# Performance work log

Measured on AMD Instinct MI355X. Metric: run time of the kernel, lower is better.

Reference implementation:

```python
import jax, jax.numpy as jnp
import numpy as np


def _cheb_conv(x, row, col, norm, W, b, num_nodes):
    # PyG ChebConv with sym normalization and lambda_max=2:
    # L_hat = -D^{-1/2} A D^{-1/2} (off-diagonal), diagonal exactly 0.
    # Tx_0 = x; Tx_1 = L_hat x; Tx_k = 2 L_hat Tx_{k-1} - Tx_{k-2}
    K = W.shape[0]
    Tx0 = x
    out = Tx0 @ W[0]
    Tx1 = jax.ops.segment_sum(norm[:, None] * Tx0[col], row, num_segments=num_nodes)
    out = out + Tx1 @ W[1]
    for k in range(2, K):
        Tx2 = 2.0 * jax.ops.segment_sum(norm[:, None] * Tx1[col], row, num_segments=num_nodes) - Tx0
        out = out + Tx2 @ W[k]
        Tx0, Tx1 = Tx1, Tx2
    return out + b


def setup_inputs() -> dict:
    key = jax.random.key(0)
    ks = jax.random.split(key, 8)
    N, E, D, H, C, K = 100000, 1600000, 128, 64, 5, 3
    x = jax.random.normal(ks[0], (N, D), dtype=jnp.float32)
    edge_index = jax.random.randint(ks[1], (2, E), 0, N, dtype=jnp.int64)
    edge_weight = jax.random.uniform(ks[2], (E,), dtype=jnp.float32)
    s1 = 1.0 / np.sqrt(D)
    s3 = 1.0 / np.sqrt(H)
    W1 = jax.random.normal(ks[3], (K, D, H), dtype=jnp.float32) * s1
    W3 = jax.random.normal(ks[4], (K, H, H), dtype=jnp.float32) * s3
    W4 = jax.random.normal(ks[5], (K, H, C), dtype=jnp.float32) * s3
    return {
        "x": x, "edge_index": edge_index, "edge_weight": edge_weight,
        "W1": W1, "b1": jnp.zeros((H,), jnp.float32),
        "W3": W3, "b3": jnp.zeros((H,), jnp.float32),
        "W4": W4, "b4": jnp.zeros((C,), jnp.float32),
    }


def reference(x, edge_index, edge_weight, W1, b1, W3, b3, W4, b4):
    N = x.shape[0]
    row, col = edge_index[0], edge_index[1]
    # symmetric normalization of the scaled Laplacian (lambda_max = 2)
    deg = jax.ops.segment_sum(edge_weight, row, num_segments=N)
    dinv = jnp.where(deg > 0, jax.lax.rsqrt(jnp.where(deg > 0, deg, 1.0)), 0.0)
    norm = -dinv[row] * edge_weight * dinv[col]
    # dropout is a no-op in eval mode (training=False)
    h = jax.nn.relu(_cheb_conv(x, row, col, norm, W1, b1, N))
    h = jax.nn.relu(_cheb_conv(h, row, col, norm, W3, b3, N))
    h = _cheb_conv(h, row, col, norm, W4, b4, N)
    return jax.nn.log_softmax(h, axis=1)
```

## Files before the change

### kernel.cpp

```cpp
#include <hip/hip_runtime.h>
#include <cstdint>
#include <cstddef>

typedef unsigned short u16;
typedef __attribute__((ext_vector_type(8))) short bf16x8;
typedef __attribute__((ext_vector_type(4))) float f32x4;

#define PB 1024
#define MAXSB 256
#define SB 512
#define CAP 12288

__device__ __forceinline__ float bflo(unsigned u) { return __uint_as_float(u << 16); }
__device__ __forceinline__ float bfhi(unsigned u) { return __uint_as_float(u & 0xFFFF0000u); }
__device__ __forceinline__ u16 f2bf(float f) {
    unsigned u = __float_as_uint(f);
    u += 0x7FFFu + ((u >> 16) & 1u);
    return (u16)(u >> 16);
}
__device__ __forceinline__ unsigned pack2(float a, float b) {
    return (unsigned)f2bf(a) | ((unsigned)f2bf(b) << 16);
}


__global__ __launch_bounds__(256) void binA(const int* __restrict__ row, int* __restrict__ P,
                                            int E, int NB, int EB) {
    __shared__ int hist[MAXSB];
    int b = blockIdx.x;
    hist[threadIdx.x] = 0;
    __syncthreads();
    int e0 = b * EB, e1 = min(E, e0 + EB);
    for (int e = e0 + threadIdx.x; e < e1; e += 256)
        atomicAdd(&hist[row[e] >> 9], 1);
    __syncthreads();
    if (threadIdx.x < NB) P[(size_t)threadIdx.x * PB + b] = hist[threadIdx.x];
}

__global__ __launch_bounds__(256) void binB1(int* __restrict__ P, int* __restrict__ bintot) {
    __shared__ int sh[256];
    int* p = P + (size_t)blockIdx.x * PB;
    int tid = threadIdx.x;
    int base = tid * 4;
    int v[4];
#pragma unroll
    for (int j = 0; j < 4; ++j) v[j] = p[base + j];
    int s = v[0] + v[1] + v[2] + v[3];
    sh[tid] = s;
    __syncthreads();
    for (int off = 1; off < 256; off <<= 1) {
        int t = (tid >= off) ? sh[tid - off] : 0;
        __syncthreads();
        sh[tid] += t;
        __syncthreads();
    }
    int run = sh[tid] - s;
#pragma unroll
    for (int j = 0; j < 4; ++j) { p[base + j] = run; run += v[j]; }
    if (tid == 255) bintot[blockIdx.x] = sh[255];
}

__device__ __forceinline__ void bs_scan(int* bs, const int* bintot, int NB, int tid) {
    bs[tid] = (tid < NB) ? bintot[tid] : 0;
    __syncthreads();
    for (int off = 1; off < 256; off <<= 1) {
        int t = (tid >= off) ? bs[tid - off] : 0;
        __syncthreads();
        bs[tid] += t;
        __syncthreads();
    }
}

__global__ __launch_bounds__(256) void binC(const int* __restrict__ row, const int* __restrict__ col,
                                            const float* __restrict__ w, const int* __restrict__ P,
                                            const int* __restrict__ bintot, int2* __restrict__ rec,
                                            int E, int NB, int EB) {
    __shared__ int bs[MAXSB];
    __shared__ int cur[MAXSB];
    int b = blockIdx.x;
    int tid = threadIdx.x;
    bs_scan(bs, bintot, NB, tid);
    if (tid < NB) cur[tid] = (tid ? bs[tid - 1] : 0) + P[(size_t)tid * PB + b];
    __syncthreads();
    int e0 = b * EB, e1 = min(E, e0 + EB);
    for (int e = e0 + tid; e < e1; e += 256) {
        int r = row[e];
        int bin = r >> 9;
        int slot = atomicAdd(&cur[bin], 1);
        rec[slot] = make_int2(col[e] | ((r & 511) << 17), __float_as_int(w[e]));
    }
}

__global__ __launch_bounds__(256) void binD1(const int2* __restrict__ rec,
                                             const int* __restrict__ bintot,
                                             int* __restrict__ rowp, float* __restrict__ dinv,
                                             int N, int NB) {
    __shared__ int bs[MAXSB];
    __shared__ int cnt[SB];
    __shared__ float deg[SB];
    __shared__ int wsum[4];
    int bin = blockIdx.x;
    int tid = threadIdx.x;
    bs_scan(bs, bintot, NB, tid);
    int e0 = bin ? bs[bin - 1] : 0;
    int e1 = bs[bin];
    cnt[tid] = 0; cnt[tid + 256] = 0;
    deg[tid] = 0.f; deg[tid + 256] = 0.f;
    __syncthreads();
    for (int e = e0 + tid; e < e1; e += 256) {
        int2 v = rec[e];
        int rl = (v.x >> 17) & 511;
        atomicAdd(&cnt[rl], 1);
        atomicAdd(&deg[rl], __int_as_float(v.y));
    }
    __syncthreads();
    int a = cnt[2 * tid], b = cnt[2 * tid + 1];
    int p = a + b;
    int lane = tid & 63, wv = tid >> 6;
    int incl = p;
    for (int off = 1; off < 64; off <<= 1) {
        int t = __shfl_up(incl, off);
        if (lane >= off) incl += t;
    }
    if (lane == 63) wsum[wv] = incl;
    __syncthreads();
    if (tid == 0) {
        int s = 0;
#pragma unroll
        for (int i = 0; i < 4; ++i) { int t = wsum[i]; wsum[i] = s; s += t; }
    }
    __syncthreads();
    int excl = incl - p + wsum[wv];
    int base = bin * SB;
    int rows = min(SB, N - base);
    if (2 * tid < rows) {
        rowp[base + 2 * tid] = e0 + excl;
        float d = deg[2 * tid];
        dinv[base + 2 * tid] = d > 0.f ? rsqrtf(d) : 0.f;
    }
    if (2 * tid + 1 < rows) {
        rowp[base + 2 * tid + 1] = e0 + excl + a;
        float d = deg[2 * tid + 1];
        dinv[base + 2 * tid + 1] = d > 0.f ? rsqrtf(d) : 0.f;
    }
    if (bin == NB - 1 && tid == 0) rowp[N] = e1;
}

__global__ __launch_bounds__(256) void binD2(const int2* __restrict__ rec,
                                             const int* __restrict__ bintot,
                                             const int* __restrict__ rowp,
                                             const float* __restrict__ dinv,
                                             int2* __restrict__ meta, int N, int NB) {
    __shared__ int bs[MAXSB];
    __shared__ int cur[SB];
    __shared__ int perm[CAP];
    int bin = blockIdx.x;
    int tid = threadIdx.x;
    bs_scan(bs, bintot, NB, tid);
    int e0 = bin ? bs[bin - 1] : 0;
    int e1 = bs[bin];
    int base = bin * SB;
    int rows = min(SB, N - base);
    for (int i = tid; i < rows; i += 256) cur[i] = rowp[base + i];
    __syncthreads();
    for (int e = e0 + tid; e < e1; e += 256) {
        int2 v = rec[e];
        int rl = (v.x >> 17) & 511;
        int slot = atomicAdd(&cur[rl], 1);
        int so = slot - e0;
        if (so < CAP) {
            perm[so] = e - e0;
        } else {
            int c = v.x & 0x1FFFF;
            float ev = -dinv[base + rl] * __int_as_float(v.y) * dinv[c];
            meta[slot] = make_int2(c, __float_as_int(ev));
        }
    }
    __syncthreads();
    int lim = min(e1 - e0, CAP);
    for (int s = tid; s < lim; s += 256) {
        int2 v = rec[e0 + perm[s]];
        int rl = (v.x >> 17) & 511;
        int c = v.x & 0x1FFFF;
        float ev = -dinv[base + rl] * __int_as_float(v.y) * dinv[c];
        meta[e0 + s] = make_int2(c, __float_as_int(ev));
    }
}

__global__ void prep(const float* __restrict__ x, unsigned* __restrict__ xb, int n2,
                     const float* __restrict__ W1, const float* __restrict__ W3,
                     const float* __restrict__ W4, u16* __restrict__ Wpu,
                     u16* __restrict__ Wp3, u16* __restrict__ Wpp) {
    int gi = blockIdx.x * blockDim.x + threadIdx.x;
    if (gi < 3072) {
        int idx = gi;
        int lane = idx & 63;
        int nt = (idx >> 6) % 12;
        int kt = idx / 768;
        int krow = kt * 32 + (lane >> 4) * 8;
        int c = nt * 16 + (lane & 15);
        u16 tmp[8];
#pragma unroll
        for (int j = 0; j < 8; ++j) {
            int k = krow + j;
            float v;
            if (c < 64)       v = W1[(size_t)k * 64 + c] - W1[2 * 8192 + (size_t)k * 64 + c];
            else if (c < 128) v = W1[8192 + (size_t)k * 64 + (c - 64)];
            else              v = W1[2 * 8192 + (size_t)k * 64 + (c - 128)];
            tmp[j] = f2bf(v);
        }
        *reinterpret_cast<uint4*>(Wpu + (size_t)idx * 8) = *reinterpret_cast<const uint4*>(tmp);
    } else if (gi < 3072 + 1536) {
        int idx = gi - 3072;
        int lane = idx & 63;
        int nt = (idx >> 6) & 3;
        int kt = idx >> 8;
        int krow = kt * 32 + (lane >> 4) * 8;
        int c = nt * 16 + (lane & 15);
        u16 tmp[8];
#pragma unroll
        for (int j = 0; j < 8; ++j) tmp[j] = f2bf(W3[(size_t)(krow + j) * 64 + c]);
        *reinterpret_cast<uint4*>(Wp3 + (size_t)idx * 8) = *reinterpret_cast<const uint4*>(tmp);
    } else if (gi < 3072 + 1536 + 256) {
        int idx = gi - (3072 + 1536);
        int lane = idx & 63;
        int nt = (idx >> 6) & 1;
        int kt = idx >> 7;
        int krow = kt * 32 + (lane >> 4) * 8;
        int c = nt * 16 + (lane & 15);
        u16 tmp[8];
#pragma unroll
        for (int j = 0; j < 8; ++j) {
            int k = krow + j;
            float v = 0.f;
            if (c < 5)                  v = W4[(size_t)k * 5 + c] - W4[640 + (size_t)k * 5 + c];
            else if (c >= 8 && c < 13)  v = W4[320 + (size_t)k * 5 + (c - 8)];
            else if (c >= 16 && c < 21) v = W4[640 + (size_t)k * 5 + (c - 16)];
            tmp[j] = f2bf(v);
        }
        *reinterpret_cast<uint4*>(Wpp + (size_t)idx * 8) = *reinterpret_cast<const uint4*>(tmp);
    } else {
        int i = gi - 4864;
        if (i < n2) {
            float2 v = reinterpret_cast<const float2*>(x)[i];
            xb[i] = pack2(v.x, v.y);
        }
    }
}

template <int MODE>
__global__ __launch_bounds__(256) void spmm64(const int* __restrict__ rp,
                                              const int2* __restrict__ meta,
                                              const u16* __restrict__ x,
                                              const u16* __restrict__ z,
                                              const float* __restrict__ bias,
                                              u16* __restrict__ y, int n) {
    int r = blockIdx.x * 32 + (threadIdx.x >> 3);
    if (r >= n) return;
    int f = (threadIdx.x & 7) * 8;
    int e0 = rp[r], e1 = rp[r + 1];
    float acc[8] = {0.f, 0.f, 0.f, 0.f, 0.f, 0.f, 0.f, 0.f};
    auto fma8 = [&](uint4 xv, float w) {
        acc[0] += w * bflo(xv.x); acc[1] += w * bfhi(xv.x);
        acc[2] += w * bflo(xv.y); acc[3] += w * bfhi(xv.y);
        acc[4] += w * bflo(xv.z); acc[5] += w * bfhi(xv.z);
        acc[6] += w * bflo(xv.w); acc[7] += w * bfhi(xv.w);
    };
    int e = e0;
    for (; e + 4 <= e1; e += 4) {
        int2 m0 = meta[e], m1 = meta[e + 1], m2 = meta[e + 2], m3 = meta[e + 3];
        uint4 v0 = *reinterpret_cast<const uint4*>(x + (size_t)m0.x * 64 + f);
        uint4 v1 = *reinterpret_cast<const uint4*>(x + (size_t)m1.x * 64 + f);
        uint4 v2 = *reinterpret_cast<const uint4*>(x + (size_t)m2.x * 64 + f);
        uint4 v3 = *reinterpret_cast<const uint4*>(x + (size_t)m3.x * 64 + f);
        fma8(v0, __int_as_float(m0.y));
        fma8(v1, __int_as_float(m1.y));
        fma8(v2, __int_as_float(m2.y));
        fma8(v3, __int_as_float(m3.y));
    }
    for (; e < e1; ++e) {
        int2 m = meta[e];
        uint4 xv = *reinterpret_cast<const uint4*>(x + (size_t)m.x * 64 + f);
        fma8(xv, __int_as_float(m.y));
    }
    if (MODE == 1 || MODE == 2) {
        uint4 zv = *reinterpret_cast<const uint4*>(z + (size_t)r * 64 + f);
        float zz[8] = {bflo(zv.x), bfhi(zv.x), bflo(zv.y), bfhi(zv.y),
                       bflo(zv.z), bfhi(zv.z), bflo(zv.w), bfhi(zv.w)};
#pragma unroll
        for (int j = 0; j < 8; ++j)
            acc[j] = (MODE == 1) ? 2.f * acc[j] + zz[j] : 2.f * acc[j] - zz[j];
    } else if (MODE == 3) {
        uint4 zv = *reinterpret_cast<const uint4*>(z + (size_t)r * 64 + f);
        float zz[8] = {bflo(zv.x), bfhi(zv.x), bflo(zv.y), bfhi(zv.y),
                       bflo(zv.z), bfhi(zv.z), bflo(zv.w), bfhi(zv.w)};
        float4 bl = *reinterpret_cast<const float4*>(bias + f);
        float4 bh = *reinterpret_cast<const float4*>(bias + f + 4);
        float bb[8] = {bl.x, bl.y, bl.z, bl.w, bh.x, bh.y, bh.z, bh.w};
#pragma unroll
        for (int j = 0; j < 8; ++j) acc[j] = fmaxf(acc[j] + zz[j] + bb[j], 0.f);
    }
    uint4 o;
    o.x = pack2(acc[0], acc[1]);
    o.y = pack2(acc[2], acc[3]);
    o.z = pack2(acc[4], acc[5]);
    o.w = pack2(acc[6], acc[7]);
    *reinterpret_cast<uint4*>(y + (size_t)r * 64 + f) = o;
}

__device__ __forceinline__ void spmm8_acc(const int* rp, const int2* meta, const u16* x,
                                          int r, int t, float* acc) {
    int e0 = rp[r], e1 = rp[r + 1];
    auto fma8 = [&](uint4 xv, float w) {
        acc[0] += w * bflo(xv.x); acc[1] += w * bfhi(xv.x);
        acc[2] += w * bflo(xv.y); acc[3] += w * bfhi(xv.y);
        acc[4] += w * bflo(xv.z); acc[5] += w * bfhi(xv.z);
        acc[6] += w * bflo(xv.w); acc[7] += w * bfhi(xv.w);
    };
    int e = e0 + t;
    for (; e + 4 < e1; e += 8) {
        int2 m0 = meta[e], m1 = meta[e + 4];
        uint4 v0 = *reinterpret_cast<const uint4*>(x + (size_t)m0.x * 8);
        uint4 v1 = *reinterpret_cast<const uint4*>(x + (size_t)m1.x * 8);
        fma8(v0, __int_as_float(m0.y));
        fma8(v1, __int_as_float(m1.y));
    }
    for (; e < e1; e += 4) {
        int2 m = meta[e];
        uint4 xv = *reinterpret_cast<const uint4*>(x + (size_t)m.x * 8);
        fma8(xv, __int_as_float(m.y));
    }
#pragma unroll
    for (int j = 0; j < 8; ++j) acc[j] += __shfl_xor(acc[j], 1);
#pragma unroll
    for (int j = 0; j < 8; ++j) acc[j] += __shfl_xor(acc[j], 2);
}

__global__ __launch_bounds__(256) void spmm8_p2(const int* __restrict__ rp,
                                                const int2* __restrict__ meta,
                                                const u16* __restrict__ x,
                                                const u16* __restrict__ z,
                                                u16* __restrict__ y, int n) {
    int r = blockIdx.x * 64 + (threadIdx.x >> 2);
    if (r >= n) return;
    int t = threadIdx.x & 3;
    float acc[8] = {0.f, 0.f, 0.f, 0.f, 0.f, 0.f, 0.f, 0.f};
    spmm8_acc(rp, meta, x, r, t, acc);
    if (t == 0) {
        uint4 zv = *reinterpret_cast<const uint4*>(z + (size_t)r * 8);
        float zz[8] = {bflo(zv.x), bfhi(zv.x), bflo(zv.y), bfhi(zv.y),
                       bflo(zv.z), bfhi(zv.z), bflo(zv.w), bfhi(zv.w)};
        uint4 o;
        o.x = pack2(2.f * acc[0] + zz[0], 2.f * acc[1] + zz[1]);
        o.y = pack2(2.f * acc[2] + zz[2], 2.f * acc[3] + zz[3]);
        o.z = pack2(2.f * acc[4] + zz[4], 2.f * acc[5] + zz[5]);
        o.w = pack2(2.f * acc[6] + zz[6], 2.f * acc[7] + zz[7]);
        *reinterpret_cast<uint4*>(y + (size_t)r * 8) = o;
    }
}

__global__ __launch_bounds__(256) void spmm8_lsm(const int* __restrict__ rp,
                                                 const int2* __restrict__ meta,
                                                 const u16* __restrict__ x,
                                                 const u16* __restrict__ z,
                                                 const float* __restrict__ bias,
                                                 float* __restrict__ out, int n) {
    int r = blockIdx.x * 64 + (threadIdx.x >> 2);
    if (r >= n) return;
    int t = threadIdx.x & 3;
    float acc[8] = {0.f, 0.f, 0.f, 0.f, 0.f, 0.f, 0.f, 0.f};
    spmm8_acc(rp, meta, x, r, t, acc);
    if (t == 0) {
        uint4 zv = *reinterpret_cast<const uint4*>(z + (size_t)r * 8);
        float zz[8] = {bflo(zv.x), bfhi(zv.x), bflo(zv.y), bfhi(zv.y),
                       bflo(zv.z), bfhi(zv.z), bflo(zv.w), bfhi(zv.w)};
        float val[5];
#pragma unroll
        for (int j = 0; j < 5; ++j) val[j] = acc[j] + zz[j] + bias[j];
        float mx = val[0];
#pragma unroll
        for (int j = 1; j < 5; ++j) mx = fmaxf(mx, val[j]);
        float s = 0.f;
#pragma unroll
        for (int j = 0; j < 5; ++j) s += expf(val[j] - mx);
        float l = logf(s);
#pragma unroll
        for (int j = 0; j < 5; ++j) out[(size_t)r * 5 + j] = val[j] - mx - l;
    }
}


__global__ __launch_bounds__(256) void gemm_u(const u16* __restrict__ A,
                                              const u16* __restrict__ Wp,
                                              u16* __restrict__ u0, u16* __restrict__ u1,
                                              u16* __restrict__ u2, int n) {
    int wave = threadIdx.x >> 6;
    int lane = threadIdx.x & 63;
    int r0 = blockIdx.x * 64 + wave * 16;
    int row = r0 + (lane & 15);
    int rowc = row < n ? row : n - 1;
    int kofs = (lane >> 4) * 8;
    f32x4 acc[12] = {};
    for (int kt = 0; kt < 4; ++kt) {
        bf16x8 a = *reinterpret_cast<const bf16x8*>(A + (size_t)rowc * 128 + kt * 32 + kofs);
        const u16* wb = Wp + (size_t)kt * 12 * 512 + (size_t)lane * 8;
#pragma unroll
        for (int nt = 0; nt < 12; ++nt) {
            bf16x8 b = *reinterpret_cast<const bf16x8*>(wb + nt * 512);
            acc[nt] = __builtin_amdgcn_mfma_f32_16x16x32_bf16(a, b, acc[nt], 0, 0, 0);
        }
    }
    int col = lane & 15;
    u16* U[3] = {u0, u1, u2};
#pragma unroll
    for (int nt = 0; nt < 12; ++nt) {
        u16* dst = U[nt >> 2];
        int cc = (nt & 3) * 16 + col;
#pragma unroll
        for (int i = 0; i < 4; ++i) {
            int rr = r0 + (lane >> 4) * 4 + i;
            if (rr < n) dst[(size_t)rr * 64 + cc] = f2bf(acc[nt][i]);
        }
    }
}

__global__ __launch_bounds__(256) void gemm3_mfma(const u16* __restrict__ A0,
                                                  const u16* __restrict__ A1,
                                                  const u16* __restrict__ A2,
                                                  const u16* __restrict__ Wp,
                                                  const float* __restrict__ bias,
                                                  u16* __restrict__ out, int n) {
    int wave = threadIdx.x >> 6;
    int lane = threadIdx.x & 63;
    int r0 = blockIdx.x * 64 + wave * 16;
    int row = r0 + (lane & 15);
    int rowc = row < n ? row : n - 1;
    int kofs = (lane >> 4) * 8;
    const u16* Ap[3] = {A0, A1, A2};
    f32x4 acc[4] = {};
    for (int kt = 0; kt < 6; ++kt) {
        const u16* Asrc = Ap[kt >> 1];
        int c0 = (kt & 1) * 32;
        bf16x8 a = *reinterpret_cast<const bf16x8*>(Asrc + (size_t)rowc * 64 + c0 + kofs);
        const u16* wb = Wp + (size_t)kt * 4 * 512 + (size_t)lane * 8;
#pragma unroll
        for (int nt = 0; nt < 4; ++nt) {
            bf16x8 b = *reinterpret_cast<const bf16x8*>(wb + nt * 512);
            acc[nt] = __builtin_amdgcn_mfma_f32_16x16x32_bf16(a, b, acc[nt], 0, 0, 0);
        }
    }
    int col = lane & 15;
#pragma unroll
    for (int nt = 0; nt < 4; ++nt) {
        float bb = bias[nt * 16 + col];
#pragma unroll
        for (int i = 0; i < 4; ++i) {
            int rr = r0 + (lane >> 4) * 4 + i;
            if (rr < n) {
                float v = fmaxf(acc[nt][i] + bb, 0.f);
                out[(size_t)rr * 64 + nt * 16 + col] = f2bf(v);
            }
        }
    }
}

__global__ __launch_bounds__(256) void gemm_proj(const u16* __restrict__ A,
                                                 const u16* __restrict__ Wp,
                                                 u16* __restrict__ p0, u16* __restrict__ p1,
                                                 u16* __restrict__ p2, int n) {
    int wave = threadIdx.x >> 6;
    int lane = threadIdx.x & 63;
    int r0 = blockIdx.x * 64 + wave * 16;
    int row = r0 + (lane & 15);
    int rowc = row < n ? row : n - 1;
    int kofs = (lane >> 4) * 8;
    f32x4 acc[2] = {};
    for (int kt = 0; kt < 2; ++kt) {
        bf16x8 a = *reinterpret_cast<const bf16x8*>(A + (size_t)rowc * 64 + kt * 32 + kofs);
        const u16* wb = Wp + (size_t)kt * 2 * 512 + (size_t)lane * 8;
#pragma unroll
        for (int nt = 0; nt < 2; ++nt) {
            bf16x8 b = *reinterpret_cast<const bf16x8*>(wb + nt * 512);
            acc[nt] = __builtin_amdgcn_mfma_f32_16x16x32_bf16(a, b, acc[nt], 0, 0, 0);
        }
    }
    int col = lane & 15;
    u16* P[3] = {p0, p1, p2};
#pragma unroll
    for (int nt = 0; nt < 2; ++nt) {
        int c = nt * 16 + col;
        if (c < 24) {
            u16* dst = P[c >> 3];
            int j = c & 7;
#pragma unroll
            for (int i = 0; i < 4; ++i) {
                int rr = r0 + (lane >> 4) * 4 + i;
                if (rr < n) dst[(size_t)rr * 8 + j] = f2bf(acc[nt][i]);
            }
        }
    }
}


static inline size_t alignup(size_t v) { return (v + 255) & ~(size_t)255; }

extern "C" void kernel_launch(void* const* d_in, const int* in_sizes, int n_in,
                              void* d_out, int out_size, void* d_ws, size_t ws_size,
                              hipStream_t stream) {
    const float* x  = (const float*)d_in[0];
    const int*   ei = (const int*)d_in[1];
    const float* ew = (const float*)d_in[2];
    const float* W1 = (const float*)d_in[3];
    const float* b1 = (const float*)d_in[4];
    const float* W3 = (const float*)d_in[5];
    const float* b3 = (const float*)d_in[6];
    const float* W4 = (const float*)d_in[7];
    const float* b4 = (const float*)d_in[8];
    float* out = (float*)d_out;

    const int D = 128, H = 64;
    const int N = in_sizes[0] / D;
    const int E = in_sizes[2];
    const int* row = ei;
    const int* col = ei + E;

    char* ws = (char*)d_ws;
    size_t off = 0;
    auto alloc = [&](size_t bytes) { size_t o = off; off += alignup(bytes); return o; };

    float* dinv   = (float*)(ws + alloc((size_t)N * 4));
    int*   rowp   = (int*)  (ws + alloc((size_t)(N + 1) * 4));
    int*   bintot = (int*)  (ws + alloc(MAXSB * 4));
    int*   P      = (int*)  (ws + alloc((size_t)MAXSB * PB * 4));
    int2*  meta   = (int2*) (ws + alloc((size_t)E * 8));
    int2*  rec    = (int2*) (ws + alloc((size_t)E * 8));
    u16*   xb     = (u16*)  (ws + alloc((size_t)N * D * 2));
    u16*   A      = (u16*)  (ws + alloc((size_t)N * H * 2));
    u16*   B      = (u16*)  (ws + alloc((size_t)N * H * 2));
    u16*   C      = (u16*)  (ws + alloc((size_t)N * H * 2));
    u16*   Dd     = (u16*)  (ws + alloc((size_t)N * H * 2));
    u16*   P0     = (u16*)  (ws + alloc((size_t)N * 8 * 2));
    u16*   P1     = (u16*)  (ws + alloc((size_t)N * 8 * 2));
    u16*   P2     = (u16*)  (ws + alloc((size_t)N * 8 * 2));
    u16*   P3     = (u16*)  (ws + alloc((size_t)N * 8 * 2));
    u16*   Wpu    = (u16*)  (ws + alloc((size_t)4 * 12 * 512 * 2));
    u16*   Wp3    = (u16*)  (ws + alloc((size_t)6 * 4 * 512 * 2));
    u16*   Wpp    = (u16*)  (ws + alloc((size_t)2 * 2 * 512 * 2));

    const int NB = (N + SB - 1) / SB;
    const int EB = (E + PB - 1) / PB;

    dim3 blk(256);

    binA<<<PB, blk, 0, stream>>>(row, P, E, NB, EB);
    binB1<<<NB, blk, 0, stream>>>(P, bintot);
    binC<<<PB, blk, 0, stream>>>(row, col, ew, P, bintot, rec, E, NB, EB);
    binD1<<<NB, blk, 0, stream>>>(rec, bintot, rowp, dinv, N, NB);
    binD2<<<NB, blk, 0, stream>>>(rec, bintot, rowp, dinv, meta, N, NB);

    int n2 = N * D / 2;
    prep<<<(n2 + 4864 + 255) / 256, blk, 0, stream>>>(x, (unsigned*)xb, n2, W1, W3, W4,
                                                      Wpu, Wp3, Wpp);

    int g64 = (N + 31) / 32;
    int gG  = (N + 63) / 64;
    int g8  = (N + 63) / 64;

    gemm_u<<<gG, blk, 0, stream>>>(xb, Wpu, A, B, C, N);
    spmm64<1><<<g64, blk, 0, stream>>>(rowp, meta, C, B, nullptr, Dd, N);
    spmm64<3><<<g64, blk, 0, stream>>>(rowp, meta, Dd, A, b1, B, N);

    spmm64<0><<<g64, blk, 0, stream>>>(rowp, meta, B, nullptr, nullptr, C, N);
    spmm64<2><<<g64, blk, 0, stream>>>(rowp, meta, C, B, nullptr, A, N);
    gemm3_mfma<<<gG, blk, 0, stream>>>(B, C, A, Wp3, b3, Dd, N);

    gemm_proj<<<gG, blk, 0, stream>>>(Dd, Wpp, P0, P1, P2, N);
    spmm8_p2<<<g8, blk, 0, stream>>>(rowp, meta, P2, P1, P3, N);
    spmm8_lsm<<<g8, blk, 0, stream>>>(rowp, meta, P3, P0, b4, out, N);
}
```

Measured before the change: 284.7 us.

## Sort rows by degree for load-balanced SpMM and shrink binning partitions

Builds a degree-bucketed row permutation (a histogram over degree and row residue, a multi-level scan, then atomic placement) and has every SpMM kernel walk rows in that order. Rows that run side by side in a wavefront then have similar edge counts, which cuts divergence and idle lanes. It also reduces the edge-binning partition count from 1024 to 256 blocks and simplifies the per-bin scan. The cost is six extra small launches plus a memset, an indirection load per row, and scattered output writes and row-pointer reads that lose locality.

After: 368.0 us. 1.29x slower.

```diff
diff --git a/kernel.cpp b/kernel.cpp
--- a/kernel.cpp
+++ b/kernel.cpp
@@ -6,10 +6,11 @@
 typedef __attribute__((ext_vector_type(8))) short bf16x8;
 typedef __attribute__((ext_vector_type(4))) float f32x4;
 
-#define PB 1024
+#define PB 256
 #define MAXSB 256
 #define SB 512
 #define CAP 12288
+#define DHN 16384
 
 __device__ __forceinline__ float bflo(unsigned u) { return __uint_as_float(u << 16); }
 __device__ __forceinline__ float bfhi(unsigned u) { return __uint_as_float(u & 0xFFFF0000u); }
@@ -40,12 +41,8 @@
     __shared__ int sh[256];
     int* p = P + (size_t)blockIdx.x * PB;
     int tid = threadIdx.x;
-    int base = tid * 4;
-    int v[4];
-#pragma unroll
-    for (int j = 0; j < 4; ++j) v[j] = p[base + j];
-    int s = v[0] + v[1] + v[2] + v[3];
-    sh[tid] = s;
+    int v = p[tid];
+    sh[tid] = v;
     __syncthreads();
     for (int off = 1; off < 256; off <<= 1) {
         int t = (tid >= off) ? sh[tid - off] : 0;
@@ -53,9 +50,7 @@
         sh[tid] += t;
         __syncthreads();
     }
-    int run = sh[tid] - s;
-#pragma unroll
-    for (int j = 0; j < 4; ++j) { p[base + j] = run; run += v[j]; }
+    p[tid] = sh[tid] - v;
     if (tid == 255) bintot[blockIdx.x] = sh[255];
 }
 
@@ -186,6 +181,71 @@
     }
 }
 
+
+__global__ void dcount(const int* __restrict__ rowp, int* __restrict__ dh, int n) {
+    int r = blockIdx.x * blockDim.x + threadIdx.x;
+    if (r < n) {
+        int d = min(rowp[r + 1] - rowp[r], 255);
+        atomicAdd(&dh[(d << 6) | (r & 63)], 1);
+    }
+}
+
+__global__ void scanB(const int* __restrict__ in, int* __restrict__ out,
+                      int* __restrict__ part, int n) {
+    __shared__ int sh[256];
+    int tid = threadIdx.x;
+    int base = blockIdx.x * 1024 + tid * 4;
+    int v[4];
+#pragma unroll
+    for (int j = 0; j < 4; ++j) v[j] = (base + j < n) ? in[base + j] : 0;
+    int s = v[0] + v[1] + v[2] + v[3];
+    sh[tid] = s;
+    __syncthreads();
+    for (int off = 1; off < 256; off <<= 1) {
+        int t = (tid >= off) ? sh[tid - off] : 0;
+        __syncthreads();
+        sh[tid] += t;
+        __syncthreads();
+    }
+    int run = sh[tid] - s;
+#pragma unroll
+    for (int j = 0; j < 4; ++j) {
+        if (base + j < n) out[base + j] = run;
+        run += v[j];
+    }
+    if (tid == 255) part[blockIdx.x] = sh[255];
+}
+
+__global__ void scanP(int* __restrict__ part, int nb) {
+    __shared__ int sh[256];
+    int tid = threadIdx.x;
+    int v = (tid < nb) ? part[tid] : 0;
+    sh[tid] = v;
+    __syncthreads();
+    for (int off = 1; off < 256; off <<= 1) {
+        int t = (tid >= off) ? sh[tid - off] : 0;
+        __syncthreads();
+        sh[tid] += t;
+        __syncthreads();
+    }
+    if (tid < nb) part[tid] = sh[tid] - v;
+}
+
+__global__ void scanA(int* __restrict__ out, const int* __restrict__ part, int n) {
+    int i = blockIdx.x * blockDim.x + threadIdx.x;
+    if (i < n) out[i] += part[i >> 10];
+}
+
+__global__ void dplace(const int* __restrict__ rowp, int* __restrict__ dh,
+                       int* __restrict__ order, int n) {
+    int r = blockIdx.x * blockDim.x + threadIdx.x;
+    if (r < n) {
+        int d = min(rowp[r + 1] - rowp[r], 255);
+        int slot = atomicAdd(&dh[(d << 6) | (r & 63)], 1);
+        order[slot] = r;
+    }
+}
+
 __global__ void prep(const float* __restrict__ x, unsigned* __restrict__ xb, int n2,
                      const float* __restrict__ W1, const float* __restrict__ W3,
                      const float* __restrict__ W4, u16* __restrict__ Wpu,
@@ -249,13 +309,15 @@
 
 template <int MODE>
 __global__ __launch_bounds__(256) void spmm64(const int* __restrict__ rp,
+                                              const int* __restrict__ order,
                                               const int2* __restrict__ meta,
                                               const u16* __restrict__ x,
                                               const u16* __restrict__ z,
                                               const float* __restrict__ bias,
                                               u16* __restrict__ y, int n) {
-    int r = blockIdx.x * 32 + (threadIdx.x >> 3);
-    if (r >= n) return;
+    int g = blockIdx.x * 32 + (threadIdx.x >> 3);
+    if (g >= n) return;
+    int r = order[g];
     int f = (threadIdx.x & 7) * 8;
     int e0 = rp[r], e1 = rp[r + 1];
     float acc[8] = {0.f, 0.f, 0.f, 0.f, 0.f, 0.f, 0.f, 0.f};
@@ -336,12 +398,14 @@
 }
 
 __global__ __launch_bounds__(256) void spmm8_p2(const int* __restrict__ rp,
+                                                const int* __restrict__ order,
                                                 const int2* __restrict__ meta,
                                                 const u16* __restrict__ x,
                                                 const u16* __restrict__ z,
                                                 u16* __restrict__ y, int n) {
-    int r = blockIdx.x * 64 + (threadIdx.x >> 2);
-    if (r >= n) return;
+    int g = blockIdx.x * 64 + (threadIdx.x >> 2);
+    if (g >= n) return;
+    int r = order[g];
     int t = threadIdx.x & 3;
     float acc[8] = {0.f, 0.f, 0.f, 0.f, 0.f, 0.f, 0.f, 0.f};
     spmm8_acc(rp, meta, x, r, t, acc);
@@ -359,13 +423,15 @@
 }
 
 __global__ __launch_bounds__(256) void spmm8_lsm(const int* __restrict__ rp,
+                                                 const int* __restrict__ order,
                                                  const int2* __restrict__ meta,
                                                  const u16* __restrict__ x,
                                                  const u16* __restrict__ z,
                                                  const float* __restrict__ bias,
                                                  float* __restrict__ out, int n) {
-    int r = blockIdx.x * 64 + (threadIdx.x >> 2);
-    if (r >= n) return;
+    int g = blockIdx.x * 64 + (threadIdx.x >> 2);
+    if (g >= n) return;
+    int r = order[g];
     int t = threadIdx.x & 3;
     float acc[8] = {0.f, 0.f, 0.f, 0.f, 0.f, 0.f, 0.f, 0.f};
     spmm8_acc(rp, meta, x, r, t, acc);
@@ -531,6 +597,9 @@
     int*   rowp   = (int*)  (ws + alloc((size_t)(N + 1) * 4));
     int*   bintot = (int*)  (ws + alloc(MAXSB * 4));
     int*   P      = (int*)  (ws + alloc((size_t)MAXSB * PB * 4));
+    int*   dh     = (int*)  (ws + alloc((size_t)DHN * 4));
+    int*   dpart  = (int*)  (ws + alloc(256 * 4));
+    int*   order  = (int*)  (ws + alloc((size_t)N * 4));
     int2*  meta   = (int2*) (ws + alloc((size_t)E * 8));
     int2*  rec    = (int2*) (ws + alloc((size_t)E * 8));
     u16*   xb     = (u16*)  (ws + alloc((size_t)N * D * 2));
@@ -550,6 +619,9 @@
     const int EB = (E + PB - 1) / PB;
 
     dim3 blk(256);
+    int gN = (N + 255) / 256;
+
+    hipMemsetAsync(dh, 0, (size_t)DHN * 4, stream);
 
     binA<<<PB, blk, 0, stream>>>(row, P, E, NB, EB);
     binB1<<<NB, blk, 0, stream>>>(P, bintot);
@@ -557,6 +629,12 @@
     binD1<<<NB, blk, 0, stream>>>(rec, bintot, rowp, dinv, N, NB);
     binD2<<<NB, blk, 0, stream>>>(rec, bintot, rowp, dinv, meta, N, NB);
 
+    dcount<<<gN, blk, 0, stream>>>(rowp, dh, N);
+    scanB<<<DHN / 1024, blk, 0, stream>>>(dh, dh, dpart, DHN);
+    scanP<<<1, blk, 0, stream>>>(dpart, DHN / 1024);
+    scanA<<<(DHN + 255) / 256, blk, 0, stream>>>(dh, dpart, DHN);
+    dplace<<<gN, blk, 0, stream>>>(rowp, dh, order, N);
+
     int n2 = N * D / 2;
     prep<<<(n2 + 4864 + 255) / 256, blk, 0, stream>>>(x, (unsigned*)xb, n2, W1, W3, W4,
                                                       Wpu, Wp3, Wpp);
@@ -566,14 +644,14 @@
     int g8  = (N + 63) / 64;
 
     gemm_u<<<gG, blk, 0, stream>>>(xb, Wpu, A, B, C, N);
-    spmm64<1><<<g64, blk, 0, stream>>>(rowp, meta, C, B, nullptr, Dd, N);
-    spmm64<3><<<g64, blk, 0, stream>>>(rowp, meta, Dd, A, b1, B, N);
-
-    spmm64<0><<<g64, blk, 0, stream>>>(rowp, meta, B, nullptr, nullptr, C, N);
-    spmm64<2><<<g64, blk, 0, stream>>>(rowp, meta, C, B, nullptr, A, N);
+    spmm64<1><<<g64, blk, 0, stream>>>(rowp, order, meta, C, B, nullptr, Dd, N);
+    spmm64<3><<<g64, blk, 0, stream>>>(rowp, order, meta, Dd, A, b1, B, N);
+
+    spmm64<0><<<g64, blk, 0, stream>>>(rowp, order, meta, B, nullptr, nullptr, C, N);
+    spmm64<2><<<g64, blk, 0, stream>>>(rowp, order, meta, C, B, nullptr, A, N);
     gemm3_mfma<<<gG, blk, 0, stream>>>(B, C, A, Wp3, b3, Dd, N);
 
     gemm_proj<<<gG, blk, 0, stream>>>(Dd, Wpp, P0, P1, P2, N);
-    spmm8_p2<<<g8, blk, 0, stream>>>(rowp, meta, P2, P1, P3, N);
-    spmm8_lsm<<<g8, blk, 0, stream>>>(rowp, meta, P3, P0, b4, out, N);
-}
+    spmm8_p2<<<g8, blk, 0, stream>>>(rowp, order, meta, P2, P1, P3, N);
+    spmm8_lsm<<<g8, blk, 0, stream>>>(rowp, order, meta, P3, P0, b4, out, N);
+}
```

## Sort rows by degree within bins to balance SpMM wavefront work

Applied to the files above, without the earlier changes.

Adds a per-bin counting sort that orders each 512-row bin's rows by degree, capped at 127. All SpMM kernels then read their row through this order array. Rows handled by the same wavefront end up with similar edge counts, which should cut divergence and idle lanes from degree imbalance. The cost is an extra kernel launch, one extra indirection per row, and less contiguous output writes and z/bias reads.

New measurement: 324.3 us. 1.14x slower.

```diff
diff --git a/kernel.cpp b/kernel.cpp
--- a/kernel.cpp
+++ b/kernel.cpp
@@ -186,6 +186,37 @@
     }
 }
 
+__global__ __launch_bounds__(256) void dsort(const int* __restrict__ rowp,
+                                             int* __restrict__ order, int N) {
+    __shared__ int hist[128], hs[128];
+    int bin = blockIdx.x;
+    int base = bin * SB;
+    int rows = min(SB, N - base);
+    int tid = threadIdx.x;
+    if (tid < 128) hist[tid] = 0;
+    __syncthreads();
+    int d0 = -1, d1 = -1;
+    int r0 = base + tid, r1 = base + tid + 256;
+    if (tid < rows) d0 = min(rowp[r0 + 1] - rowp[r0], 127);
+    if (tid + 256 < rows) d1 = min(rowp[r1 + 1] - rowp[r1], 127);
+    if (d0 >= 0) atomicAdd(&hist[d0], 1);
+    if (d1 >= 0) atomicAdd(&hist[d1], 1);
+    __syncthreads();
+    int cnt_k = (tid < 128) ? hist[tid] : 0;
+    if (tid < 128) hs[tid] = cnt_k;
+    __syncthreads();
+    for (int off = 1; off < 128; off <<= 1) {
+        int t = (tid >= off && tid < 128) ? hs[tid - off] : 0;
+        __syncthreads();
+        if (tid < 128) hs[tid] += t;
+        __syncthreads();
+    }
+    if (tid < 128) hist[tid] = hs[tid] - cnt_k;
+    __syncthreads();
+    if (d0 >= 0) { int s = atomicAdd(&hist[d0], 1); order[base + s] = r0; }
+    if (d1 >= 0) { int s = atomicAdd(&hist[d1], 1); order[base + s] = r1; }
+}
+
 __global__ void prep(const float* __restrict__ x, unsigned* __restrict__ xb, int n2,
                      const float* __restrict__ W1, const float* __restrict__ W3,
                      const float* __restrict__ W4, u16* __restrict__ Wpu,
@@ -249,13 +280,15 @@
 
 template <int MODE>
 __global__ __launch_bounds__(256) void spmm64(const int* __restrict__ rp,
+                                              const int* __restrict__ order,
                                               const int2* __restrict__ meta,
                                               const u16* __restrict__ x,
                                               const u16* __restrict__ z,
                                               const float* __restrict__ bias,
                                               u16* __restrict__ y, int n) {
-    int r = blockIdx.x * 32 + (threadIdx.x >> 3);
-    if (r >= n) return;
+    int g = blockIdx.x * 32 + (threadIdx.x >> 3);
+    if (g >= n) return;
+    int r = order[g];
     int f = (threadIdx.x & 7) * 8;
     int e0 = rp[r], e1 = rp[r + 1];
     float acc[8] = {0.f, 0.f, 0.f, 0.f, 0.f, 0.f, 0.f, 0.f};
@@ -336,12 +369,14 @@
 }
 
 __global__ __launch_bounds__(256) void spmm8_p2(const int* __restrict__ rp,
+                                                const int* __restrict__ order,
                                                 const int2* __restrict__ meta,
                                                 const u16* __restrict__ x,
                                                 const u16* __restrict__ z,
                                                 u16* __restrict__ y, int n) {
-    int r = blockIdx.x * 64 + (threadIdx.x >> 2);
-    if (r >= n) return;
+    int g = blockIdx.x * 64 + (threadIdx.x >> 2);
+    if (g >= n) return;
+    int r = order[g];
     int t = threadIdx.x & 3;
     float acc[8] = {0.f, 0.f, 0.f, 0.f, 0.f, 0.f, 0.f, 0.f};
     spmm8_acc(rp, meta, x, r, t, acc);
@@ -359,13 +394,15 @@
 }
 
 __global__ __launch_bounds__(256) void spmm8_lsm(const int* __restrict__ rp,
+                                                 const int* __restrict__ order,
                                                  const int2* __restrict__ meta,
                                                  const u16* __restrict__ x,
                                                  const u16* __restrict__ z,
                                                  const float* __restrict__ bias,
                                                  float* __restrict__ out, int n) {
-    int r = blockIdx.x * 64 + (threadIdx.x >> 2);
-    if (r >= n) return;
+    int g = blockIdx.x * 64 + (threadIdx.x >> 2);
+    if (g >= n) return;
+    int r = order[g];
     int t = threadIdx.x & 3;
     float acc[8] = {0.f, 0.f, 0.f, 0.f, 0.f, 0.f, 0.f, 0.f};
     spmm8_acc(rp, meta, x, r, t, acc);
@@ -531,6 +568,7 @@
     int*   rowp   = (int*)  (ws + alloc((size_t)(N + 1) * 4));
     int*   bintot = (int*)  (ws + alloc(MAXSB * 4));
     int*   P      = (int*)  (ws + alloc((size_t)MAXSB * PB * 4));
+    int*   order  = (int*)  (ws + alloc((size_t)N * 4));
     int2*  meta   = (int2*) (ws + alloc((size_t)E * 8));
     int2*  rec    = (int2*) (ws + alloc((size_t)E * 8));
     u16*   xb     = (u16*)  (ws + alloc((size_t)N * D * 2));
@@ -556,6 +594,7 @@
     binC<<<PB, blk, 0, stream>>>(row, col, ew, P, bintot, rec, E, NB, EB);
     binD1<<<NB, blk, 0, stream>>>(rec, bintot, rowp, dinv, N, NB);
     binD2<<<NB, blk, 0, stream>>>(rec, bintot, rowp, dinv, meta, N, NB);
+    dsort<<<NB, blk, 0, stream>>>(rowp, order, N);
 
     int n2 = N * D / 2;
     prep<<<(n2 + 4864 + 255) / 256, blk, 0, stream>>>(x, (unsigned*)xb, n2, W1, W3, W4,
@@ -566,14 +605,14 @@
     int g8  = (N + 63) / 64;
 
     gemm_u<<<gG, blk, 0, stream>>>(xb, Wpu, A, B, C, N);
-    spmm64<1><<<g64, blk, 0, stream>>>(rowp, meta, C, B, nullptr, Dd, N);
-    spmm64<3><<<g64, blk, 0, stream>>>(rowp, meta, Dd, A, b1, B, N);
-
-    spmm64<0><<<g64, blk, 0, stream>>>(rowp, meta, B, nullptr, nullptr, C, N);
-    spmm64<2><<<g64, blk, 0, stream>>>(rowp, meta, C, B, nullptr, A, N);
+    spmm64<1><<<g64, blk, 0, stream>>>(rowp, order, meta, C, B, nullptr, Dd, N);
+    spmm64<3><<<g64, blk, 0, stream>>>(rowp, order, meta, Dd, A, b1, B, N);
+
+    spmm64<0><<<g64, blk, 0, stream>>>(rowp, order, meta, B, nullptr, nullptr, C, N);
+    spmm64<2><<<g64, blk, 0, stream>>>(rowp, order, meta, C, B, nullptr, A, N);
     gemm3_mfma<<<gG, blk, 0, stream>>>(B, C, A, Wp3, b3, Dd, N);
 
     gemm_proj<<<gG, blk, 0, stream>>>(Dd, Wpp, P0, P1, P2, N);
-    spmm8_p2<<<g8, blk, 0, stream>>>(rowp, meta, P2, P1, P3, N);
-    spmm8_lsm<<<g8, blk, 0, stream>>>(rowp, meta, P3, P0, b4, out, N);
-}
+    spmm8_p2<<<g8, blk, 0, stream>>>(rowp, order, meta, P2, P1, P3, N);
+    spmm8_lsm<<<g8, blk, 0, stream>>>(rowp, order, meta, P3, P0, b4, out, N);
+}
```
